# Performance work log

Measured on AMD Instinct MI355X. Metric: run time of the kernel, lower is better.

The kernel has to match this reference:

```python
import jax, jax.numpy as jnp
import numpy as np
from jax import lax

EPS = 1e-7  # keras.backend.epsilon()
DT = 0.05

def _k(a):
    # (3,3) -> HWIO (3,3,1,1) fp32 kernel constant
    return jnp.asarray(np.asarray(a, dtype=np.float32).reshape(3, 3, 1, 1))

KXP = _k([[0,0,0],[0,-1,1],[0,0,0]])
KXN = _k([[0,0,0],[-1,1,0],[0,0,0]])
KYP = _k([[0,1,0],[0,-1,0],[0,0,0]])
KYN = _k([[0,0,0],[0,1,0],[0,-1,0]])
KXC = _k([[0,0,0],[-1,0,1],[0,0,0]])
KYC = _k([[0,1,0],[0,0,0],[0,-1,0]])
KLX = _k([[1,0,-1],[2,0,-2],[1,0,-1]])
KLY = _k([[1,2,1],[0,0,0],[-1,-2,-1]])

def conv(x, k):
    # TF K.conv2d 'same' == XLA cross-correlation, NHWC/HWIO
    return lax.conv_general_dilated(x, k, (1, 1), 'SAME',
                                    dimension_numbers=('NHWC', 'HWIO', 'NHWC'))

def setup_inputs() -> dict:
    key = jax.random.key(0)
    k1, k2 = jax.random.split(key)
    B, H, W = 32, 512, 512
    u = jax.random.normal(k1, (B, H, W, 1), dtype=jnp.float32)
    img = jax.random.uniform(k2, (B, H, W, 1), dtype=jnp.float32)
    alpha = jnp.ones((1, 1, 1, 1), jnp.float32)
    beta = jnp.ones((1, 1, 1, 1), jnp.float32)
    gamma = jnp.ones((1, 1, 1, 1), jnp.float32)
    return {"u": u, "img": img, "alpha": alpha, "beta": beta, "gamma": gamma}

def reference(u, img, alpha, beta, gamma):
    # --- edge stopping function g(img) (precomputed in build() in original) ---
    ex = conv(img, KLX)
    ey = conv(img, KLY)
    edges = jnp.square(jnp.square(ex) + jnp.square(ey))
    edges = edges / jnp.max(edges)
    edges = 1.0 / (edges + 1.0)
    gex = conv(edges, KXC)
    gey = conv(edges, KYC)
    # --- upwind transport term ---
    xp = conv(u, KXP); xn = conv(u, KXN)
    yp = conv(u, KYP); yn = conv(u, KYN)
    fxp = jax.nn.relu(gex); fxn = -jax.nn.relu(-gex)
    fyp = jax.nn.relu(gey); fyn = -jax.nn.relu(-gey)
    transport = 20.0 * ((fxp * xp + fxn * xn) + (fyp * yp + fyn * yn))
    # --- curvature (divergence of normalized gradient) ---
    gux = conv(u, KXC)
    guy = conv(u, KYC)
    normu = jnp.sqrt(jnp.square(gux) + jnp.square(guy) + EPS)
    kappa = conv(gux / (normu + EPS), KXC) + conv(guy / (normu + EPS), KYC)
    curvature = edges * kappa * normu
    balloon = edges * normu
    return u + DT * (curvature * alpha + transport * beta + balloon * gamma)
```

## Files before the change

### kernel.cpp

```cpp
#include <hip/hip_runtime.h>

#define HH 512
#define WW 512
#define NB 32
#define EPSF 1e-7f
#define DTF 0.05f
#define RS1 8
#define RSF 8

__device__ __forceinline__ float bperm(int addr, float v) {
    return __int_as_float(__builtin_amdgcn_ds_bpermute(addr, __float_as_int(v)));
}

struct R10 { float v[10]; };

__device__ __forceinline__ void load_row10(const float* __restrict__ base, int row,
                                           int lane, int bpu, int bpd,
                                           bool lo, bool hi, R10& r) {
    if ((unsigned)row < (unsigned)HH) {
        const float4* p = (const float4*)(base + row * WW + 8 * lane);
        float4 a = p[0], b = p[1];
        r.v[1] = a.x; r.v[2] = a.y; r.v[3] = a.z; r.v[4] = a.w;
        r.v[5] = b.x; r.v[6] = b.y; r.v[7] = b.z; r.v[8] = b.w;
    } else {
        #pragma unroll
        for (int k = 1; k <= 8; ++k) r.v[k] = 0.f;
    }
    float l = bperm(bpu, r.v[8]);
    float h = bperm(bpd, r.v[1]);
    r.v[0] = lo ? 0.f : l;
    r.v[9] = hi ? 0.f : h;
}

__global__ __launch_bounds__(256, 2)
void max_e4_kernel(const float* __restrict__ img, float* __restrict__ partial) {
    const int wid  = blockIdx.x * 4 + (threadIdx.x >> 6);
    const int lane = threadIdx.x & 63;
    const int rs = wid & 63;
    const int b  = wid >> 6;
    const int i0 = rs * RS1;
    const float* __restrict__ IM = img + (size_t)b * (HH * WW);
    const bool lo = (lane == 0), hi = (lane == 63);
    const int bpu = ((lane + 63) & 63) << 2, bpd = ((lane + 1) & 63) << 2;

    R10 A, B, C;
    load_row10(IM, i0 - 1, lane, bpu, bpd, lo, hi, A);
    load_row10(IM, i0,     lane, bpu, bpd, lo, hi, B);
    float m = 0.f;
    #pragma unroll
    for (int i = i0; i < i0 + RS1; ++i) {
        load_row10(IM, i + 1, lane, bpu, bpd, lo, hi, C);
        #pragma unroll
        for (int k = 1; k <= 8; ++k) {
            float ex = (A.v[k-1] - A.v[k+1]) + 2.f * (B.v[k-1] - B.v[k+1]) + (C.v[k-1] - C.v[k+1]);
            float ey = (A.v[k-1] - C.v[k-1]) + 2.f * (A.v[k] - C.v[k]) + (A.v[k+1] - C.v[k+1]);
            float s2 = ex * ex + ey * ey;
            m = fmaxf(m, s2 * s2);
        }
        A = B; B = C;
    }
    for (int off = 32; off > 0; off >>= 1)
        m = fmaxf(m, __shfl_down(m, off, 64));
    if (lane == 0) partial[wid] = m;
}

__global__ __launch_bounds__(256)
void reduce_max(const float* __restrict__ partial, float* __restrict__ wsmax) {
    float v = 0.f;
    #pragma unroll
    for (int k = 0; k < 8; ++k)
        v = fmaxf(v, partial[threadIdx.x + 256 * k]);
    for (int off = 32; off > 0; off >>= 1)
        v = fmaxf(v, __shfl_down(v, off, 64));
    __shared__ float smax[4];
    const int lane = threadIdx.x & 63, w = threadIdx.x >> 6;
    if (lane == 0) smax[w] = v;
    __syncthreads();
    if (threadIdx.x == 0)
        wsmax[0] = fmaxf(fmaxf(smax[0], smax[1]), fmaxf(smax[2], smax[3]));
}

__global__ __launch_bounds__(256, 2)
void fused_ff(const float* __restrict__ u, const float* __restrict__ img,
              const float* __restrict__ pa, const float* __restrict__ pb,
              const float* __restrict__ pg, const float* __restrict__ wsmax,
              float* __restrict__ out) {
    const int wid  = blockIdx.x * 4 + (threadIdx.x >> 6);
    const int lane = threadIdx.x & 63;
    const int rs = wid & 63;
    const int b  = wid >> 6;
    const int o0 = rs * RSF;
    const size_t base = (size_t)b * (HH * WW);
    const float* __restrict__ U  = u + base;
    const float* __restrict__ IM = img + base;
    float* __restrict__ O = out + base;
    const bool lo = (lane == 0), hi = (lane == 63);
    const int bpu = ((lane + 63) & 63) << 2, bpd = ((lane + 1) & 63) << 2;

    const float M   = wsmax[0];
    const float dta = DTF * pa[0];
    const float dtb = 20.f * DTF * pb[0];
    const float dtg = DTF * pg[0];

    R10 I0 = {}, I1 = {}, R1 = {}, R2 = {}, E2 = {}, PX2 = {};
    float R0[9] = {}, E1[9] = {}, PY1[9] = {}, PY2[9] = {};

    if (o0 >= 2) {
        load_row10(IM, o0 - 2, lane, bpu, bpd, lo, hi, I0);
        load_row10(IM, o0 - 1, lane, bpu, bpd, lo, hi, I1);
        load_row10(U,  o0 - 2, lane, bpu, bpd, lo, hi, R1);
        load_row10(U,  o0 - 1, lane, bpu, bpd, lo, hi, R2);
    }

    #pragma unroll
    for (int o = o0 - 2; o < o0 + RSF; ++o) {
        R10 C, W;
        load_row10(IM, o + 2, lane, bpu, bpd, lo, hi, C);
        load_row10(U,  o + 2, lane, bpu, bpd, lo, hi, W);

        float eN[10], PXN[10], PYN[9];
        if (o >= -1 && o < HH - 1) {
            #pragma unroll
            for (int k = 1; k <= 8; ++k) {
                float ex = (I0.v[k-1] - I0.v[k+1]) + 2.f * (I1.v[k-1] - I1.v[k+1]) + (C.v[k-1] - C.v[k+1]);
                float ey = (I0.v[k-1] - C.v[k-1]) + 2.f * (I0.v[k] - C.v[k]) + (I0.v[k+1] - C.v[k+1]);
                float s2 = ex * ex + ey * ey;
                eN[k] = M * __builtin_amdgcn_rcpf(s2 * s2 + M);
                float gux = R2.v[k+1] - R2.v[k-1];
                float guy = R1.v[k] - W.v[k];
                float rn  = __builtin_amdgcn_rsqf(gux * gux + guy * guy + EPSF);
                PXN[k] = gux * rn;
                PYN[k] = guy * rn;
            }
        } else {
            #pragma unroll
            for (int k = 1; k <= 8; ++k) { eN[k] = 0.f; PXN[k] = 0.f; PYN[k] = 0.f; }
        }
        {
            float a = bperm(bpu, eN[8]),  bb = bperm(bpd, eN[1]);
            float c = bperm(bpu, PXN[8]), d  = bperm(bpd, PXN[1]);
            eN[0]  = lo ? 0.f : a;  eN[9]  = hi ? 0.f : bb;
            PXN[0] = lo ? 0.f : c;  PXN[9] = hi ? 0.f : d;
        }

        if (o >= o0) {
            float vals[8];
            #pragma unroll
            for (int k = 1; k <= 8; ++k) {
                float gex = E2.v[k+1] - E2.v[k-1];
                float gey = E1[k] - eN[k];
                float xp = R1.v[k+1] - R1.v[k], xn = R1.v[k] - R1.v[k-1];
                float yp = R0[k] - R1.v[k],     yn = R1.v[k] - R2.v[k];
                float tr = fmaxf(gex, 0.f) * xp + fminf(gex, 0.f) * xn
                         + fmaxf(gey, 0.f) * yp + fminf(gey, 0.f) * yn;
                float gxc = R1.v[k+1] - R1.v[k-1], gyc = R0[k] - R2.v[k];
                float ncv = __builtin_amdgcn_sqrtf(gxc * gxc + gyc * gyc + EPSF);
                float kap = (PX2.v[k+1] - PX2.v[k-1]) + (PY1[k] - PYN[k]);
                vals[k-1] = R1.v[k] + E2.v[k] * ncv * (kap * dta + dtg) + tr * dtb;
            }
            float4* p = (float4*)(O + o * WW + 8 * lane);
            p[0] = make_float4(vals[0], vals[1], vals[2], vals[3]);
            p[1] = make_float4(vals[4], vals[5], vals[6], vals[7]);
        }

        I0 = I1; I1 = C;
        #pragma unroll
        for (int k = 1; k <= 8; ++k) { R0[k] = R1.v[k]; E1[k] = E2.v[k]; PY1[k] = PY2[k]; PY2[k] = PYN[k]; }
        R1 = R2; R2 = W;
        E2 = *(R10*)&eN[0]; PX2 = *(R10*)&PXN[0];
    }
}

extern "C" void kernel_launch(void* const* d_in, const int* in_sizes, int n_in,
                              void* d_out, int out_size, void* d_ws, size_t ws_size,
                              hipStream_t stream) {
    const float* u   = (const float*)d_in[0];
    const float* img = (const float*)d_in[1];
    const float* pa  = (const float*)d_in[2];
    const float* pb  = (const float*)d_in[3];
    const float* pg  = (const float*)d_in[4];
    float* out = (float*)d_out;
    float* partial = (float*)d_ws;
    float* wsmax   = partial + 2048;

    max_e4_kernel<<<512, 256, 0, stream>>>(img, partial);
    reduce_max<<<1, 256, 0, stream>>>(partial, wsmax);
    fused_ff<<<512, 256, 0, stream>>>(u, img, pa, pb, pg, wsmax, out);
}
```

Measured before the change: 125.0 us.

## Shrink row strips, raise occupancy, and specialize edge strips without bounds checks

```diff
diff --git a/kernel.cpp b/kernel.cpp
--- a/kernel.cpp
+++ b/kernel.cpp
@@ -5,8 +5,8 @@
 #define NB 32
 #define EPSF 1e-7f
 #define DTF 0.05f
-#define RS1 8
-#define RSF 8
+#define RS1 2
+#define RSF 4
 
 __device__ __forceinline__ float bperm(int addr, float v) {
     return __int_as_float(__builtin_amdgcn_ds_bpermute(addr, __float_as_int(v)));
@@ -14,42 +14,36 @@
 
 struct R10 { float v[10]; };
 
+template<bool EDGE>
 __device__ __forceinline__ void load_row10(const float* __restrict__ base, int row,
                                            int lane, int bpu, int bpd,
                                            bool lo, bool hi, R10& r) {
-    if ((unsigned)row < (unsigned)HH) {
-        const float4* p = (const float4*)(base + row * WW + 8 * lane);
-        float4 a = p[0], b = p[1];
-        r.v[1] = a.x; r.v[2] = a.y; r.v[3] = a.z; r.v[4] = a.w;
-        r.v[5] = b.x; r.v[6] = b.y; r.v[7] = b.z; r.v[8] = b.w;
-    } else {
-        #pragma unroll
-        for (int k = 1; k <= 8; ++k) r.v[k] = 0.f;
-    }
+    int rc = row;
+    if (EDGE) rc = min(max(row, 0), HH - 1);
+    const float4* p = (const float4*)(base + rc * WW + 8 * lane);
+    float4 a = p[0], b = p[1];
+    if (EDGE && ((unsigned)row >= (unsigned)HH)) {
+        a.x = a.y = a.z = a.w = 0.f;
+        b.x = b.y = b.z = b.w = 0.f;
+    }
+    r.v[1] = a.x; r.v[2] = a.y; r.v[3] = a.z; r.v[4] = a.w;
+    r.v[5] = b.x; r.v[6] = b.y; r.v[7] = b.z; r.v[8] = b.w;
     float l = bperm(bpu, r.v[8]);
     float h = bperm(bpd, r.v[1]);
     r.v[0] = lo ? 0.f : l;
     r.v[9] = hi ? 0.f : h;
 }
 
-__global__ __launch_bounds__(256, 2)
-void max_e4_kernel(const float* __restrict__ img, float* __restrict__ partial) {
-    const int wid  = blockIdx.x * 4 + (threadIdx.x >> 6);
-    const int lane = threadIdx.x & 63;
-    const int rs = wid & 63;
-    const int b  = wid >> 6;
-    const int i0 = rs * RS1;
-    const float* __restrict__ IM = img + (size_t)b * (HH * WW);
-    const bool lo = (lane == 0), hi = (lane == 63);
-    const int bpu = ((lane + 63) & 63) << 2, bpd = ((lane + 1) & 63) << 2;
-
+template<bool EDGE>
+__device__ __forceinline__ float e4_strip(const float* __restrict__ IM, int i0,
+                                          int lane, int bpu, int bpd, bool lo, bool hi) {
     R10 A, B, C;
-    load_row10(IM, i0 - 1, lane, bpu, bpd, lo, hi, A);
-    load_row10(IM, i0,     lane, bpu, bpd, lo, hi, B);
+    load_row10<EDGE>(IM, i0 - 1, lane, bpu, bpd, lo, hi, A);
+    load_row10<EDGE>(IM, i0,     lane, bpu, bpd, lo, hi, B);
     float m = 0.f;
     #pragma unroll
     for (int i = i0; i < i0 + RS1; ++i) {
-        load_row10(IM, i + 1, lane, bpu, bpd, lo, hi, C);
+        load_row10<EDGE>(IM, i + 1, lane, bpu, bpd, lo, hi, C);
         #pragma unroll
         for (int k = 1; k <= 8; ++k) {
             float ex = (A.v[k-1] - A.v[k+1]) + 2.f * (B.v[k-1] - B.v[k+1]) + (C.v[k-1] - C.v[k+1]);
@@ -59,6 +53,24 @@
         }
         A = B; B = C;
     }
+    return m;
+}
+
+__global__ __launch_bounds__(256, 6)
+void max_e4_kernel(const float* __restrict__ img, float* __restrict__ partial) {
+    const int wid  = blockIdx.x * 4 + (threadIdx.x >> 6);
+    const int lane = threadIdx.x & 63;
+    const int rs = wid & 255;
+    const int b  = wid >> 8;
+    const int i0 = rs * RS1;
+    const float* __restrict__ IM = img + (size_t)b * (HH * WW);
+    const bool lo = (lane == 0), hi = (lane == 63);
+    const int bpu = ((lane + 63) & 63) << 2, bpd = ((lane + 1) & 63) << 2;
+
+    float m = (rs == 0 || rs == 255)
+        ? e4_strip<true >(IM, i0, lane, bpu, bpd, lo, hi)
+        : e4_strip<false>(IM, i0, lane, bpu, bpd, lo, hi);
+
     for (int off = 32; off > 0; off >>= 1)
         m = fmaxf(m, __shfl_down(m, off, 64));
     if (lane == 0) partial[wid] = m;
@@ -66,10 +78,13 @@
 
 __global__ __launch_bounds__(256)
 void reduce_max(const float* __restrict__ partial, float* __restrict__ wsmax) {
+    const float4* p4 = (const float4*)partial;
     float v = 0.f;
     #pragma unroll
-    for (int k = 0; k < 8; ++k)
-        v = fmaxf(v, partial[threadIdx.x + 256 * k]);
+    for (int k = 0; k < 8; ++k) {
+        float4 a = p4[threadIdx.x + 256 * k];
+        v = fmaxf(v, fmaxf(fmaxf(a.x, a.y), fmaxf(a.z, a.w)));
+    }
     for (int off = 32; off > 0; off >>= 1)
         v = fmaxf(v, __shfl_down(v, off, 64));
     __shared__ float smax[4];
@@ -80,67 +95,48 @@
         wsmax[0] = fmaxf(fmaxf(smax[0], smax[1]), fmaxf(smax[2], smax[3]));
 }
 
-__global__ __launch_bounds__(256, 2)
-void fused_ff(const float* __restrict__ u, const float* __restrict__ img,
-              const float* __restrict__ pa, const float* __restrict__ pb,
-              const float* __restrict__ pg, const float* __restrict__ wsmax,
-              float* __restrict__ out) {
-    const int wid  = blockIdx.x * 4 + (threadIdx.x >> 6);
-    const int lane = threadIdx.x & 63;
-    const int rs = wid & 63;
-    const int b  = wid >> 6;
-    const int o0 = rs * RSF;
-    const size_t base = (size_t)b * (HH * WW);
-    const float* __restrict__ U  = u + base;
-    const float* __restrict__ IM = img + base;
-    float* __restrict__ O = out + base;
-    const bool lo = (lane == 0), hi = (lane == 63);
-    const int bpu = ((lane + 63) & 63) << 2, bpd = ((lane + 1) & 63) << 2;
-
-    const float M   = wsmax[0];
-    const float dta = DTF * pa[0];
-    const float dtb = 20.f * DTF * pb[0];
-    const float dtg = DTF * pg[0];
-
-    R10 I0 = {}, I1 = {}, R1 = {}, R2 = {}, E2 = {}, PX2 = {};
+template<bool EDGE>
+__device__ __forceinline__ void ff_impl(const float* __restrict__ U,
+                                        const float* __restrict__ IM,
+                                        float* __restrict__ O,
+                                        int o0, int lane, int bpu, int bpd,
+                                        bool lo, bool hi, float M,
+                                        float dta, float dtb, float dtg) {
+    R10 I0, I1, R1, R2, E2 = {}, PX2 = {};
     float R0[9] = {}, E1[9] = {}, PY1[9] = {}, PY2[9] = {};
 
-    if (o0 >= 2) {
-        load_row10(IM, o0 - 2, lane, bpu, bpd, lo, hi, I0);
-        load_row10(IM, o0 - 1, lane, bpu, bpd, lo, hi, I1);
-        load_row10(U,  o0 - 2, lane, bpu, bpd, lo, hi, R1);
-        load_row10(U,  o0 - 1, lane, bpu, bpd, lo, hi, R2);
-    }
+    load_row10<EDGE>(IM, o0 - 2, lane, bpu, bpd, lo, hi, I0);
+    load_row10<EDGE>(IM, o0 - 1, lane, bpu, bpd, lo, hi, I1);
+    load_row10<EDGE>(U,  o0 - 2, lane, bpu, bpd, lo, hi, R1);
+    load_row10<EDGE>(U,  o0 - 1, lane, bpu, bpd, lo, hi, R2);
 
     #pragma unroll
     for (int o = o0 - 2; o < o0 + RSF; ++o) {
         R10 C, W;
-        load_row10(IM, o + 2, lane, bpu, bpd, lo, hi, C);
-        load_row10(U,  o + 2, lane, bpu, bpd, lo, hi, W);
-
-        float eN[10], PXN[10], PYN[9];
-        if (o >= -1 && o < HH - 1) {
-            #pragma unroll
-            for (int k = 1; k <= 8; ++k) {
-                float ex = (I0.v[k-1] - I0.v[k+1]) + 2.f * (I1.v[k-1] - I1.v[k+1]) + (C.v[k-1] - C.v[k+1]);
-                float ey = (I0.v[k-1] - C.v[k-1]) + 2.f * (I0.v[k] - C.v[k]) + (I0.v[k+1] - C.v[k+1]);
-                float s2 = ex * ex + ey * ey;
-                eN[k] = M * __builtin_amdgcn_rcpf(s2 * s2 + M);
-                float gux = R2.v[k+1] - R2.v[k-1];
-                float guy = R1.v[k] - W.v[k];
-                float rn  = __builtin_amdgcn_rsqf(gux * gux + guy * guy + EPSF);
-                PXN[k] = gux * rn;
-                PYN[k] = guy * rn;
-            }
-        } else {
-            #pragma unroll
-            for (int k = 1; k <= 8; ++k) { eN[k] = 0.f; PXN[k] = 0.f; PYN[k] = 0.f; }
+        load_row10<EDGE>(IM, o + 2, lane, bpu, bpd, lo, hi, C);
+        load_row10<EDGE>(U,  o + 2, lane, bpu, bpd, lo, hi, W);
+
+        R10 eN, PXN;
+        float PYN[9];
+        const bool zrow = EDGE && (o < -1 || o >= HH - 1);
+        #pragma unroll
+        for (int k = 1; k <= 8; ++k) {
+            float ex = (I0.v[k-1] - I0.v[k+1]) + 2.f * (I1.v[k-1] - I1.v[k+1]) + (C.v[k-1] - C.v[k+1]);
+            float ey = (I0.v[k-1] - C.v[k-1]) + 2.f * (I0.v[k] - C.v[k]) + (I0.v[k+1] - C.v[k+1]);
+            float s2 = ex * ex + ey * ey;
+            float e  = M * __builtin_amdgcn_rcpf(s2 * s2 + M);
+            float gux = R2.v[k+1] - R2.v[k-1];
+            float guy = R1.v[k] - W.v[k];
+            float rn  = __builtin_amdgcn_rsqf(gux * gux + guy * guy + EPSF);
+            eN.v[k]  = zrow ? 0.f : e;
+            PXN.v[k] = zrow ? 0.f : gux * rn;
+            PYN[k]   = zrow ? 0.f : guy * rn;
         }
         {
-            float a = bperm(bpu, eN[8]),  bb = bperm(bpd, eN[1]);
-            float c = bperm(bpu, PXN[8]), d  = bperm(bpd, PXN[1]);
-            eN[0]  = lo ? 0.f : a;  eN[9]  = hi ? 0.f : bb;
-            PXN[0] = lo ? 0.f : c;  PXN[9] = hi ? 0.f : d;
+            float a = bperm(bpu, eN.v[8]),  bb = bperm(bpd, eN.v[1]);
+            float c = bperm(bpu, PXN.v[8]), d  = bperm(bpd, PXN.v[1]);
+            eN.v[0]  = lo ? 0.f : a;  eN.v[9]  = hi ? 0.f : bb;
+            PXN.v[0] = lo ? 0.f : c;  PXN.v[9] = hi ? 0.f : d;
         }
 
         if (o >= o0) {
@@ -148,7 +144,7 @@
             #pragma unroll
             for (int k = 1; k <= 8; ++k) {
                 float gex = E2.v[k+1] - E2.v[k-1];
-                float gey = E1[k] - eN[k];
+                float gey = E1[k] - eN.v[k];
                 float xp = R1.v[k+1] - R1.v[k], xn = R1.v[k] - R1.v[k-1];
                 float yp = R0[k] - R1.v[k],     yn = R1.v[k] - R2.v[k];
                 float tr = fmaxf(gex, 0.f) * xp + fminf(gex, 0.f) * xn
@@ -167,8 +163,33 @@
         #pragma unroll
         for (int k = 1; k <= 8; ++k) { R0[k] = R1.v[k]; E1[k] = E2.v[k]; PY1[k] = PY2[k]; PY2[k] = PYN[k]; }
         R1 = R2; R2 = W;
-        E2 = *(R10*)&eN[0]; PX2 = *(R10*)&PXN[0];
-    }
+        E2 = eN; PX2 = PXN;
+    }
+}
+
+__global__ __launch_bounds__(256, 3)
+void fused_ff(const float* __restrict__ u, const float* __restrict__ img,
+              const float* __restrict__ pa, const float* __restrict__ pb,
+              const float* __restrict__ pg, const float* __restrict__ wsmax,
+              float* __restrict__ out) {
+    const int wid  = blockIdx.x * 4 + (threadIdx.x >> 6);
+    const int lane = threadIdx.x & 63;
+    const int rs = wid & 127;
+    const int b  = wid >> 7;
+    const int o0 = rs * RSF;
+    const size_t base = (size_t)b * (HH * WW);
+    const bool lo = (lane == 0), hi = (lane == 63);
+    const int bpu = ((lane + 63) & 63) << 2, bpd = ((lane + 1) & 63) << 2;
+
+    const float M   = wsmax[0];
+    const float dta = DTF * pa[0];
+    const float dtb = 20.f * DTF * pb[0];
+    const float dtg = DTF * pg[0];
+
+    if (rs == 0 || rs == 127)
+        ff_impl<true >(u + base, img + base, out + base, o0, lane, bpu, bpd, lo, hi, M, dta, dtb, dtg);
+    else
+        ff_impl<false>(u + base, img + base, out + base, o0, lane, bpu, bpd, lo, hi, M, dta, dtb, dtg);
 }
 
 extern "C" void kernel_launch(void* const* d_in, const int* in_sizes, int n_in,
@@ -181,9 +202,9 @@
     const float* pg  = (const float*)d_in[4];
     float* out = (float*)d_out;
     float* partial = (float*)d_ws;
-    float* wsmax   = partial + 2048;
-
-    max_e4_kernel<<<512, 256, 0, stream>>>(img, partial);
+    float* wsmax   = partial + 8192;
+
+    max_e4_kernel<<<2048, 256, 0, stream>>>(img, partial);
     reduce_max<<<1, 256, 0, stream>>>(partial, wsmax);
-    fused_ff<<<512, 256, 0, stream>>>(u, img, pa, pb, pg, wsmax, out);
-}
+    fused_ff<<<1024, 256, 0, stream>>>(u, img, pa, pb, pg, wsmax, out);
+}
```

After: 174.9 us. +40.0%, slower.
